# Kernel optimization log

Hardware: AMD Instinct MI355X
Metric: run time of the kernel (lower is better)

The kernel has to match this reference:

```python
import jax, jax.numpy as jnp
import numpy as np

B, S, H, NH = 2, 2048, 512, 8
DK = H // NH


def setup_inputs() -> dict:
    key = jax.random.key(0)
    ks = jax.random.split(key, 12)
    inp = {
        "query": jax.random.normal(ks[0], (B, S, H), dtype=jnp.float32),
        "key": jax.random.normal(ks[1], (B, S, H), dtype=jnp.float32),
        "value": jax.random.normal(ks[2], (B, S, H), dtype=jnp.float32),
        "bias": jax.random.normal(ks[3], (B, 1, S, S), dtype=jnp.float32),
        "mask": jax.random.randint(ks[4], (B, S), 0, 2, dtype=jnp.int32),
        "Wq": jax.random.normal(ks[5], (H, H), dtype=jnp.float32) * 0.02,
        "bq": jax.random.normal(ks[6], (H,), dtype=jnp.float32) * 0.02,
        "Wk": jax.random.normal(ks[7], (H, H), dtype=jnp.float32) * 0.02,
        "bk": jax.random.normal(ks[8], (H,), dtype=jnp.float32) * 0.02,
        "Wv": jax.random.normal(ks[9], (H, H), dtype=jnp.float32) * 0.02,
        "bv": jax.random.normal(ks[10], (H,), dtype=jnp.float32) * 0.02,
    }
    return inp


def reference(query, key, value, bias, mask, Wq, bq, Wk, bk, Wv, bv):
    b = query.shape[0]
    # torch nn.Linear: x @ W.T + b, then split heads -> [B, h, S, d_k]
    def proj(x, W, bb):
        y = x @ W.T + bb
        return y.reshape(b, -1, NH, DK).transpose(0, 2, 1, 3)

    q = proj(query, Wq, bq)
    k = proj(key, Wk, bk)
    v = proj(value, Wv, bv)

    score = jnp.einsum("bhqd,bhkd->bhqk", q, k) / np.sqrt(DK).astype(np.float32)
    # NOTE: the source swaps bias/mask when calling attention():
    #   the 0/1 mask is ADDED to the scores...
    mask_add = mask.reshape(b, 1, 1, -1).astype(score.dtype)
    score = score + mask_add
    #   ...and the float bias is used for the masked_fill (bias == 0 -> -1e30).
    score = jnp.where(bias == 0, jnp.asarray(-1e30, score.dtype), score)
    attn = jax.nn.softmax(score, axis=-1)  # dropout=None in the source call
    x = jnp.einsum("bhqk,bhkd->bhqd", attn, v)
    return x.transpose(0, 2, 1, 3).reshape(b, -1, NH * DK)
```

## Files before the change

kernel.cpp:

```cpp
#include <hip/hip_runtime.h>
#include <hip/hip_bf16.h>
#include <stdint.h>

#define B_  2
#define S_  2048
#define H_  512
#define NH_ 8
#define DK_ 64

typedef __bf16 bf16x8 __attribute__((ext_vector_type(8)));
typedef short  s16x4  __attribute__((ext_vector_type(4)));
typedef float  f32x4  __attribute__((ext_vector_type(4)));

static __device__ __forceinline__ uint32_t pk2(float a, float b) {
  __hip_bfloat162 h = __float22bfloat162_rn(float2{a, b});
  uint32_t u;
  __builtin_memcpy(&u, &h, 4);
  return u;
}
static __device__ __forceinline__ uint4 pkf8(float4 a, float4 b) {
  return uint4{pk2(a.x, a.y), pk2(a.z, a.w), pk2(b.x, b.y), pk2(b.z, b.w)};
}

static __device__ __forceinline__ f32x4 mfma_k16(s16x4 a, s16x4 b, f32x4 c) {
#if defined(__HIP_DEVICE_COMPILE__)
  return __builtin_amdgcn_mfma_f32_16x16x16bf16_1k(a, b, c, 0, 0, 0);
#else
  (void)a; (void)b;
  return c;
#endif
}

typedef const __attribute__((address_space(1))) uint32_t* gas_t;
typedef __attribute__((address_space(3))) uint32_t* las_t;
static __device__ __forceinline__ void cp16(const void* g, void* l) {
  __builtin_amdgcn_global_load_lds((gas_t)g, (las_t)l, 16, 0, 0);
}

__global__ __launch_bounds__(256) void prep_kernel(const float* __restrict__ bias,
                                                   const int* __restrict__ mask,
                                                   uint32_t* __restrict__ zc,
                                                   float* __restrict__ fmL) {
  int bid = blockIdx.x, t = threadIdx.x;
  if (bid < 4096) {
    size_t tid = (size_t)bid * 256 + t;
    const uint4* src = (const uint4*)(bias + tid * 8);
    uint4 a = src[0], b2 = src[1];
    bool z = ((a.x << 1) == 0u) | ((a.y << 1) == 0u) |
             ((a.z << 1) == 0u) | ((a.w << 1) == 0u) |
             ((b2.x << 1) == 0u) | ((b2.y << 1) == 0u) |
             ((b2.z << 1) == 0u) | ((b2.w << 1) == 0u);
    if (z) {
      size_t flat = tid * 8;
      int bb = (int)(flat >> 22);
      int q  = (int)(flat >> 11) & 2047;
      int k  = (int)flat & 2047;
      atomicOr(&zc[(bb * 32 + (q >> 6)) * 32 + (k >> 6)], 1u);
    }
  } else {
    const float LOG2E = 1.44269504088896340736f;
#pragma unroll
    for (int i = 0; i < 16; i++) {
      int idx = i * 256 + t;
      fmL[idx] = (float)mask[idx] * LOG2E;
    }
  }
}

struct ProjArgs {
  const float* X[3];
  const float* W[3];
  const float* Bv[3];
  uint16_t*    O[3];
};

__global__ __launch_bounds__(256) void proj_kernel(ProjArgs pa) {
  int bid = blockIdx.x;
  int mat = bid >> 8;
  int rem = bid & 255;
  int mtile = rem >> 3, dtile = rem & 7;
  int m0 = mtile * 128, n0 = dtile * 64;
  const float* X  = pa.X[mat];
  const float* Wt = pa.W[mat];
  const float* Bv = pa.Bv[mat];
  uint16_t*    O  = pa.O[mat];

  __shared__ uint16_t Xs[128][64];
  __shared__ uint16_t Ws[64][64];

  int t = threadIdx.x;
  int w = t >> 6, l = t & 63, lo = l & 15, g = l >> 4;
  int srow = t >> 1, shalf = t & 1;
  int wrow = t >> 2, wq = t & 3;

  const float* Xrow = X + (size_t)(m0 + srow) * 512 + shalf * 32;
  const float* Wrow = Wt + (size_t)(n0 + wrow) * 512 + wq * 16;

  f32x4 acc[2][4];
#pragma unroll
  for (int st = 0; st < 2; st++)
#pragma unroll
    for (int dt = 0; dt < 4; dt++) acc[st][dt] = (f32x4){0.f, 0.f, 0.f, 0.f};

  float4 xa[8], wa2[4];
  {
    const float4* sx = (const float4*)Xrow;
    const float4* sw = (const float4*)Wrow;
#pragma unroll
    for (int i = 0; i < 8; i++) xa[i] = sx[i];
#pragma unroll
    for (int i = 0; i < 4; i++) wa2[i] = sw[i];
  }

  for (int kb = 0; kb < 8; kb++) {
#pragma unroll
    for (int j = 0; j < 4; j++) {
      int s = (shalf * 4 + j) ^ (srow & 7);
      *(uint4*)&Xs[srow][s * 8] = pkf8(xa[2 * j], xa[2 * j + 1]);
    }
#pragma unroll
    for (int j = 0; j < 2; j++) {
      int s = (wq * 2 + j) ^ (wrow & 7);
      *(uint4*)&Ws[wrow][s * 8] = pkf8(wa2[2 * j], wa2[2 * j + 1]);
    }
    __syncthreads();
    if (kb < 7) {
      const float4* sx = (const float4*)(Xrow + (kb + 1) * 64);
      const float4* sw = (const float4*)(Wrow + (kb + 1) * 64);
#pragma unroll
      for (int i = 0; i < 8; i++) xa[i] = sx[i];
#pragma unroll
      for (int i = 0; i < 4; i++) wa2[i] = sw[i];
    }
#pragma unroll
    for (int kk = 0; kk < 2; kk++) {
      int seg = (kk * 4 + g) ^ (lo & 7);
      bf16x8 xf[2], wf[4];
#pragma unroll
      for (int st = 0; st < 2; st++)
        xf[st] = *(const bf16x8*)&Xs[w * 32 + st * 16 + lo][seg * 8];
#pragma unroll
      for (int dt = 0; dt < 4; dt++)
        wf[dt] = *(const bf16x8*)&Ws[dt * 16 + lo][seg * 8];
      if (mat < 2) {
#pragma unroll
        for (int st = 0; st < 2; st++)
#pragma unroll
          for (int dt = 0; dt < 4; dt++)
            acc[st][dt] = __builtin_amdgcn_mfma_f32_16x16x32_bf16(wf[dt], xf[st], acc[st][dt], 0, 0, 0);
      } else {
#pragma unroll
        for (int st = 0; st < 2; st++)
#pragma unroll
          for (int dt = 0; dt < 4; dt++)
            acc[st][dt] = __builtin_amdgcn_mfma_f32_16x16x32_bf16(xf[st], wf[dt], acc[st][dt], 0, 0, 0);
      }
    }
    __syncthreads();
  }

  if (mat < 2) {
    float scale = (mat == 0) ? 0.125f : 1.0f;
    float4 bv4[4];
#pragma unroll
    for (int dt = 0; dt < 4; dt++)
      bv4[dt] = *(const float4*)(Bv + n0 + dt * 16 + g * 4);
#pragma unroll
    for (int st = 0; st < 2; st++) {
      int ss = m0 + w * 32 + st * 16 + lo;
      int bb = ss >> 11, sIn = ss & 2047;
      uint16_t* obase = O + ((size_t)(bb * NH_ + dtile) * S_ + sIn) * DK_;
#pragma unroll
      for (int dt = 0; dt < 4; dt++) {
        float v0 = (acc[st][dt][0] + bv4[dt].x) * scale;
        float v1 = (acc[st][dt][1] + bv4[dt].y) * scale;
        float v2 = (acc[st][dt][2] + bv4[dt].z) * scale;
        float v3 = (acc[st][dt][3] + bv4[dt].w) * scale;
        uint2 pk{pk2(v0, v1), pk2(v2, v3)};
        *(uint2*)(obase + dt * 16 + g * 4) = pk;
      }
    }
  } else {
    float bval[4];
#pragma unroll
    for (int dt = 0; dt < 4; dt++) bval[dt] = Bv[n0 + dt * 16 + lo];
#pragma unroll
    for (int st = 0; st < 2; st++) {
      int m = m0 + w * 32 + st * 16 + g * 4;
      int bb = m >> 11, sIn = m & 2047;
#pragma unroll
      for (int dt = 0; dt < 4; dt++) {
        int dd = dt * 16 + lo;
        float v0 = acc[st][dt][0] + bval[dt];
        float v1 = acc[st][dt][1] + bval[dt];
        float v2 = acc[st][dt][2] + bval[dt];
        float v3 = acc[st][dt][3] + bval[dt];
        uint2 pk{pk2(v0, v1), pk2(v2, v3)};
        *(uint2*)(O + ((size_t)(bb * NH_ + dtile) * DK_ + dd) * S_ + sIn) = pk;
      }
    }
  }
}

__global__ __launch_bounds__(256, 2) void attn_kernel(
    const uint16_t* __restrict__ Qb, const uint16_t* __restrict__ Kb,
    const uint16_t* __restrict__ Vt, const uint32_t* __restrict__ zc,
    const float* __restrict__ fmL, const float* __restrict__ bias,
    float* __restrict__ out) {
  int bid = blockIdx.x;
  int bh = bid & 15, qtile = bid >> 4;
  int b = bh >> 3, h = bh & 7;
  int q0 = qtile * 64;
  int t = threadIdx.x;
  int w = t >> 6, l = t & 63, lo = l & 15, g = l >> 4;

  __shared__ __align__(16) char smem[32768];
  uint16_t* KsB = (uint16_t*)smem;
  uint16_t* VsB = (uint16_t*)(smem + 16384);

  const uint16_t* Qh = Qb + (size_t)bh * S_ * DK_;
  const uint16_t* Kh = Kb + (size_t)bh * S_ * DK_;
  const uint16_t* Vh = Vt + (size_t)bh * DK_ * S_;

  int lrow = l >> 3, lseg = (l & 7) ^ (lrow & 7);
  const uint16_t* kbase = Kh + (size_t)(w * 16 + lrow) * DK_ + lseg * 8;
  const uint16_t* vbase = Vh + (size_t)(w * 16 + lrow) * S_ + lseg * 8;
  uint16_t* kd0 = KsB + (w * 16) * 64;
  uint16_t* kd8 = KsB + (w * 16 + 8) * 64;
  uint16_t* vd0 = VsB + (w * 16) * 64;
  uint16_t* vd8 = VsB + (w * 16 + 8) * 64;

  bf16x8 qf[4][2];
#pragma unroll
  for (int qt = 0; qt < 4; qt++)
#pragma unroll
    for (int kk = 0; kk < 2; kk++)
      qf[qt][kk] = *(const bf16x8*)(Qh + (size_t)(q0 + qt * 16 + lo) * DK_ + kk * 32 + g * 8);

  f32x4 o[4][4];
#pragma unroll
  for (int dt = 0; dt < 4; dt++)
#pragma unroll
    for (int qt = 0; qt < 4; qt++) o[dt][qt] = (f32x4){0.f, 0.f, 0.f, 0.f};
  float ts[4] = {0.f, 0.f, 0.f, 0.f};

  const uint32_t* zcr = zc + ((b * 32 + qtile) << 5);
  const float* fmrow = fmL + b * S_ + w * 16 + g * 4;
  const float LOG2E = 1.44269504088896340736f;

  cp16(kbase, kd0);
  cp16(kbase + 512, kd8);
  cp16(vbase, vd0);
  cp16(vbase + 8 * S_, vd8);

  for (int kb = 0; kb < 32; kb++) {
    int cur = kb & 1;
    int k0 = kb * 64;
    float4 mv4 = *(const float4*)(fmrow + k0);
    uint32_t zci = zcr[kb];
    __syncthreads();
    if (kb + 1 < 32) {
      int kn = k0 + 64;
      int nb = (cur ^ 1) * 4096;
      cp16(kbase + (size_t)kn * 64, kd0 + nb);
      cp16(kbase + (size_t)kn * 64 + 512, kd8 + nb);
      cp16(vbase + kn, vd0 + nb);
      cp16(vbase + kn + 8 * S_, vd8 + nb);
    }
    const uint16_t* KsT = KsB + cur * 4096;
    const uint16_t* VsT = VsB + cur * 4096;

    s16x4 vf[4];
    {
      int s = (2 * w + (g >> 1)) ^ (lo & 7);
      int off = s * 8 + (g & 1) * 4;
#pragma unroll
      for (int dt = 0; dt < 4; dt++)
        vf[dt] = *(const s16x4*)(VsT + (dt * 16 + lo) * 64 + off);
    }
    bf16x8 kf[2];
#pragma unroll
    for (int kk = 0; kk < 2; kk++) {
      int s = (kk * 4 + g) ^ (lo & 7);
      kf[kk] = *(const bf16x8*)(KsT + (w * 16 + lo) * 64 + s * 8);
    }

    f32x4 c[4];
#pragma unroll
    for (int qt = 0; qt < 4; qt++) {
      f32x4 z = {0.f, 0.f, 0.f, 0.f};
      z = __builtin_amdgcn_mfma_f32_16x16x32_bf16(kf[0], qf[qt][0], z, 0, 0, 0);
      c[qt] = __builtin_amdgcn_mfma_f32_16x16x32_bf16(kf[1], qf[qt][1], z, 0, 0, 0);
    }

    float p[4][4];
    if (zci == 0u) {
#pragma unroll
      for (int qt = 0; qt < 4; qt++) {
        p[qt][0] = __builtin_amdgcn_exp2f(__builtin_fmaf(c[qt][0], LOG2E, mv4.x));
        p[qt][1] = __builtin_amdgcn_exp2f(__builtin_fmaf(c[qt][1], LOG2E, mv4.y));
        p[qt][2] = __builtin_amdgcn_exp2f(__builtin_fmaf(c[qt][2], LOG2E, mv4.z));
        p[qt][3] = __builtin_amdgcn_exp2f(__builtin_fmaf(c[qt][3], LOG2E, mv4.w));
      }
    } else {
#pragma unroll
      for (int qt = 0; qt < 4; qt++) {
        float4 bz = *(const float4*)(bias + ((size_t)(b * S_ + q0 + qt * 16 + lo)) * S_ + k0 + w * 16 + g * 4);
        p[qt][0] = (bz.x == 0.f) ? 0.f : __builtin_amdgcn_exp2f(__builtin_fmaf(c[qt][0], LOG2E, mv4.x));
        p[qt][1] = (bz.y == 0.f) ? 0.f : __builtin_amdgcn_exp2f(__builtin_fmaf(c[qt][1], LOG2E, mv4.y));
        p[qt][2] = (bz.z == 0.f) ? 0.f : __builtin_amdgcn_exp2f(__builtin_fmaf(c[qt][2], LOG2E, mv4.z));
        p[qt][3] = (bz.w == 0.f) ? 0.f : __builtin_amdgcn_exp2f(__builtin_fmaf(c[qt][3], LOG2E, mv4.w));
      }
    }

    s16x4 pf[4];
#pragma unroll
    for (int qt = 0; qt < 4; qt++) {
      ts[qt] += (p[qt][0] + p[qt][1]) + (p[qt][2] + p[qt][3]);
      union { s16x4 v; uint32_t u[2]; } uu;
      uu.u[0] = pk2(p[qt][0], p[qt][1]);
      uu.u[1] = pk2(p[qt][2], p[qt][3]);
      pf[qt] = uu.v;
    }

#pragma unroll
    for (int dt = 0; dt < 4; dt++)
#pragma unroll
      for (int qt = 0; qt < 4; qt++)
        o[dt][qt] = mfma_k16(vf[dt], pf[qt], o[dt][qt]);
  }

  float* OT = (float*)smem;
  float* LS = (float*)(smem + 17408);
#pragma unroll
  for (int qt = 0; qt < 4; qt++) {
    float v = ts[qt];
    v += __shfl_xor(v, 16);
    v += __shfl_xor(v, 32);
    ts[qt] = v;
  }
  __syncthreads();
  if (g == 0) {
#pragma unroll
    for (int qt = 0; qt < 4; qt++) LS[(w * 4 + qt) * 16 + lo] = ts[qt];
  }
#pragma unroll
  for (int ww = 0; ww < 4; ww++) {
    if (w == ww) {
#pragma unroll
      for (int dt = 0; dt < 4; dt++)
#pragma unroll
        for (int qt = 0; qt < 4; qt++)
#pragma unroll
          for (int r = 0; r < 4; r++) {
            int idx = (dt * 16 + g * 4 + r) * 68 + qt * 16 + lo;
            if (ww == 0) OT[idx] = o[dt][qt][r];
            else         OT[idx] += o[dt][qt][r];
          }
    }
    __syncthreads();
  }
  {
    int q = t >> 2, dseg = (t & 3) * 16;
    int qt2 = q >> 4, lo2 = q & 15;
    float lsum = LS[(0 * 4 + qt2) * 16 + lo2] + LS[(1 * 4 + qt2) * 16 + lo2] +
                 LS[(2 * 4 + qt2) * 16 + lo2] + LS[(3 * 4 + qt2) * 16 + lo2];
    float linv = 1.0f / fmaxf(lsum, 1e-30f);
    float* ob = out + ((size_t)(b * S_ + q0 + q)) * H_ + h * DK_ + dseg;
#pragma unroll
    for (int i = 0; i < 4; i++) {
      float4 v;
      v.x = OT[(dseg + i * 4 + 0) * 68 + q] * linv;
      v.y = OT[(dseg + i * 4 + 1) * 68 + q] * linv;
      v.z = OT[(dseg + i * 4 + 2) * 68 + q] * linv;
      v.w = OT[(dseg + i * 4 + 3) * 68 + q] * linv;
      *(float4*)(ob + i * 4) = v;
    }
  }
}

extern "C" void kernel_launch(void* const* d_in, const int* in_sizes, int n_in,
                              void* d_out, int out_size, void* d_ws, size_t ws_size,
                              hipStream_t stream) {
  const float* query = (const float*)d_in[0];
  const float* key   = (const float*)d_in[1];
  const float* value = (const float*)d_in[2];
  const float* bias  = (const float*)d_in[3];
  const int*   mask  = (const int*)d_in[4];
  const float* Wq = (const float*)d_in[5];
  const float* bq = (const float*)d_in[6];
  const float* Wk = (const float*)d_in[7];
  const float* bk = (const float*)d_in[8];
  const float* Wv = (const float*)d_in[9];
  const float* bv = (const float*)d_in[10];

  char* ws = (char*)d_ws;
  uint32_t* zcflags = (uint32_t*)ws;
  float*    fmL     = (float*)(ws + 8192);
  uint16_t* Qb = (uint16_t*)(ws + (size_t)(1 << 20));
  uint16_t* Kb = (uint16_t*)(ws + (size_t)(5 << 20));
  uint16_t* Vt = (uint16_t*)(ws + (size_t)(9 << 20));

  (void)hipMemsetAsync(zcflags, 0, 8192, stream);
  prep_kernel<<<4097, 256, 0, stream>>>(bias, mask, zcflags, fmL);

  ProjArgs pa;
  pa.X[0] = query; pa.X[1] = key; pa.X[2] = value;
  pa.W[0] = Wq;    pa.W[1] = Wk;  pa.W[2] = Wv;
  pa.Bv[0] = bq;   pa.Bv[1] = bk; pa.Bv[2] = bv;
  pa.O[0] = Qb;    pa.O[1] = Kb;  pa.O[2] = Vt;
  proj_kernel<<<768, 256, 0, stream>>>(pa);

  attn_kernel<<<512, 256, 0, stream>>>(Qb, Kb, Vt, zcflags, fmL, bias, (float*)d_out);
}
```

Baseline: 179.4 us.

## Fuse bias-zero scan into projection kernel and double attention key tile per block

Merges the bias-zero scan and mask prep into the projection launch, and drops the memset and atomics. Zero flags are now stored as per-row bitmasks built with wave ballots, then OR-reduced per query tile inside attention. The attention kernel moves to 512 threads that process 128-key blocks with larger LDS double buffers and a two-bank output reduction. This cuts launch count and per-iteration sync overhead, at the cost of 64KB of LDS per block and coarser zero-skip granularity (128 keys).

```diff
diff --git a/kernel.cpp b/kernel.cpp
--- a/kernel.cpp
+++ b/kernel.cpp
@@ -37,46 +37,54 @@
   __builtin_amdgcn_global_load_lds((gas_t)g, (las_t)l, 16, 0, 0);
 }
 
-__global__ __launch_bounds__(256) void prep_kernel(const float* __restrict__ bias,
-                                                   const int* __restrict__ mask,
-                                                   uint32_t* __restrict__ zc,
-                                                   float* __restrict__ fmL) {
-  int bid = blockIdx.x, t = threadIdx.x;
-  if (bid < 4096) {
-    size_t tid = (size_t)bid * 256 + t;
-    const uint4* src = (const uint4*)(bias + tid * 8);
-    uint4 a = src[0], b2 = src[1];
-    bool z = ((a.x << 1) == 0u) | ((a.y << 1) == 0u) |
-             ((a.z << 1) == 0u) | ((a.w << 1) == 0u) |
-             ((b2.x << 1) == 0u) | ((b2.y << 1) == 0u) |
-             ((b2.z << 1) == 0u) | ((b2.w << 1) == 0u);
-    if (z) {
-      size_t flat = tid * 8;
-      int bb = (int)(flat >> 22);
-      int q  = (int)(flat >> 11) & 2047;
-      int k  = (int)flat & 2047;
-      atomicOr(&zc[(bb * 32 + (q >> 6)) * 32 + (k >> 6)], 1u);
-    }
-  } else {
-    const float LOG2E = 1.44269504088896340736f;
-#pragma unroll
-    for (int i = 0; i < 16; i++) {
-      int idx = i * 256 + t;
-      fmL[idx] = (float)mask[idx] * LOG2E;
-    }
-  }
-}
-
 struct ProjArgs {
   const float* X[3];
   const float* W[3];
   const float* Bv[3];
   uint16_t*    O[3];
+  const float* bias;
+  const int*   mask;
+  uint32_t*    zrow;
+  float*       fmL;
 };
 
-__global__ __launch_bounds__(256) void proj_kernel(ProjArgs pa) {
-  int bid = blockIdx.x;
-  int mat = bid >> 8;
+__global__ __launch_bounds__(256) void prep_proj_kernel(ProjArgs pa) {
+  __shared__ __align__(16) char psm[24640];
+  int bid = blockIdx.x, t = threadIdx.x;
+
+  if (bid >= 768) {
+    if (bid < 4864) {
+      int r = bid - 768;
+      uint32_t* wbuf = (uint32_t*)psm;
+      const uint4* src = (const uint4*)(pa.bias + (size_t)r * 2048 + t * 8);
+      uint4 a = src[0], b2 = src[1];
+      bool z = ((a.x << 1) == 0u) | ((a.y << 1) == 0u) |
+               ((a.z << 1) == 0u) | ((a.w << 1) == 0u) |
+               ((b2.x << 1) == 0u) | ((b2.y << 1) == 0u) |
+               ((b2.z << 1) == 0u) | ((b2.w << 1) == 0u);
+      uint64_t m = __ballot(z);
+      if ((t & 63) == 0) {
+        uint32_t bits = 0;
+#pragma unroll
+        for (int c = 0; c < 8; c++)
+          bits |= (uint32_t)(((m >> (8 * c)) & 0xFFull) != 0ull) << c;
+        wbuf[t >> 6] = bits;
+      }
+      __syncthreads();
+      if (t == 0)
+        pa.zrow[r] = wbuf[0] | (wbuf[1] << 8) | (wbuf[2] << 16) | (wbuf[3] << 24);
+    } else {
+      const float LOG2E = 1.44269504088896340736f;
+#pragma unroll
+      for (int i = 0; i < 16; i++) {
+        int idx = i * 256 + t;
+        pa.fmL[idx] = (float)pa.mask[idx] * LOG2E;
+      }
+    }
+    return;
+  }
+
+  int mat = bid / 256;
   int rem = bid & 255;
   int mtile = rem >> 3, dtile = rem & 7;
   int m0 = mtile * 128, n0 = dtile * 64;
@@ -85,10 +93,9 @@
   const float* Bv = pa.Bv[mat];
   uint16_t*    O  = pa.O[mat];
 
-  __shared__ uint16_t Xs[128][64];
-  __shared__ uint16_t Ws[64][64];
-
-  int t = threadIdx.x;
+  uint16_t (*Xs)[64] = (uint16_t (*)[64])psm;
+  uint16_t (*Ws)[64] = (uint16_t (*)[64])(psm + 16384);
+
   int w = t >> 6, l = t & 63, lo = l & 15, g = l >> 4;
   int srow = t >> 1, shalf = t & 1;
   int wrow = t >> 2, wq = t & 3;
@@ -202,9 +209,9 @@
   }
 }
 
-__global__ __launch_bounds__(256, 2) void attn_kernel(
+__global__ __launch_bounds__(512, 4) void attn_kernel(
     const uint16_t* __restrict__ Qb, const uint16_t* __restrict__ Kb,
-    const uint16_t* __restrict__ Vt, const uint32_t* __restrict__ zc,
+    const uint16_t* __restrict__ Vt, const uint32_t* __restrict__ zrow,
     const float* __restrict__ fmL, const float* __restrict__ bias,
     float* __restrict__ out) {
   int bid = blockIdx.x;
@@ -214,21 +221,28 @@
   int t = threadIdx.x;
   int w = t >> 6, l = t & 63, lo = l & 15, g = l >> 4;
 
-  __shared__ __align__(16) char smem[32768];
+  __shared__ __align__(16) char smem[65536];
   uint16_t* KsB = (uint16_t*)smem;
-  uint16_t* VsB = (uint16_t*)(smem + 16384);
+  uint16_t* VsB = (uint16_t*)(smem + 32768);
 
   const uint16_t* Qh = Qb + (size_t)bh * S_ * DK_;
   const uint16_t* Kh = Kb + (size_t)bh * S_ * DK_;
   const uint16_t* Vh = Vt + (size_t)bh * DK_ * S_;
 
-  int lrow = l >> 3, lseg = (l & 7) ^ (lrow & 7);
+  int lrow = l >> 3, lseg = (l & 7) ^ lrow;
   const uint16_t* kbase = Kh + (size_t)(w * 16 + lrow) * DK_ + lseg * 8;
-  const uint16_t* vbase = Vh + (size_t)(w * 16 + lrow) * S_ + lseg * 8;
   uint16_t* kd0 = KsB + (w * 16) * 64;
   uint16_t* kd8 = KsB + (w * 16 + 8) * 64;
-  uint16_t* vd0 = VsB + (w * 16) * 64;
-  uint16_t* vd8 = VsB + (w * 16 + 8) * 64;
+  int vrow0 = w * 4 + (l >> 4);
+  int vrow1 = 32 + w * 4 + (l >> 4);
+  const uint16_t* vb0 = Vh + (size_t)vrow0 * S_ + (((l & 15) ^ (vrow0 & 15)) * 8);
+  const uint16_t* vb1 = Vh + (size_t)vrow1 * S_ + (((l & 15) ^ (vrow1 & 15)) * 8);
+  uint16_t* vd0 = VsB + (w * 4) * 128;
+  uint16_t* vd1 = VsB + (32 + w * 4) * 128;
+
+  uint32_t zall = zrow[(b << 11) + q0 + l];
+#pragma unroll
+  for (int s = 1; s < 64; s <<= 1) zall |= __shfl_xor(zall, s);
 
   bf16x8 qf[4][2];
 #pragma unroll
@@ -244,45 +258,44 @@
     for (int qt = 0; qt < 4; qt++) o[dt][qt] = (f32x4){0.f, 0.f, 0.f, 0.f};
   float ts[4] = {0.f, 0.f, 0.f, 0.f};
 
-  const uint32_t* zcr = zc + ((b * 32 + qtile) << 5);
   const float* fmrow = fmL + b * S_ + w * 16 + g * 4;
   const float LOG2E = 1.44269504088896340736f;
 
   cp16(kbase, kd0);
-  cp16(kbase + 512, kd8);
-  cp16(vbase, vd0);
-  cp16(vbase + 8 * S_, vd8);
-
-  for (int kb = 0; kb < 32; kb++) {
+  cp16(kbase + 8 * DK_, kd8);
+  cp16(vb0, vd0);
+  cp16(vb1, vd1);
+
+  for (int kb = 0; kb < 16; kb++) {
     int cur = kb & 1;
-    int k0 = kb * 64;
+    int k0 = kb * 128;
     float4 mv4 = *(const float4*)(fmrow + k0);
-    uint32_t zci = zcr[kb];
     __syncthreads();
-    if (kb + 1 < 32) {
-      int kn = k0 + 64;
-      int nb = (cur ^ 1) * 4096;
-      cp16(kbase + (size_t)kn * 64, kd0 + nb);
-      cp16(kbase + (size_t)kn * 64 + 512, kd8 + nb);
-      cp16(vbase + kn, vd0 + nb);
-      cp16(vbase + kn + 8 * S_, vd8 + nb);
-    }
-    const uint16_t* KsT = KsB + cur * 4096;
-    const uint16_t* VsT = VsB + cur * 4096;
+    if (kb + 1 < 16) {
+      int kn = k0 + 128;
+      int nb = (cur ^ 1) * 8192;
+      cp16(kbase + (size_t)kn * DK_, kd0 + nb);
+      cp16(kbase + (size_t)kn * DK_ + 8 * DK_, kd8 + nb);
+      cp16(vb0 + kn, vd0 + nb);
+      cp16(vb1 + kn, vd1 + nb);
+    }
+    const uint16_t* KsT = KsB + cur * 8192;
+    const uint16_t* VsT = VsB + cur * 8192;
 
     s16x4 vf[4];
     {
-      int s = (2 * w + (g >> 1)) ^ (lo & 7);
-      int off = s * 8 + (g & 1) * 4;
-#pragma unroll
-      for (int dt = 0; dt < 4; dt++)
-        vf[dt] = *(const s16x4*)(VsT + (dt * 16 + lo) * 64 + off);
+      int sl = 2 * w + (g >> 1);
+#pragma unroll
+      for (int dt = 0; dt < 4; dt++) {
+        int sp = sl ^ lo;
+        vf[dt] = *(const s16x4*)(VsT + (dt * 16 + lo) * 128 + sp * 8 + (g & 1) * 4);
+      }
     }
     bf16x8 kf[2];
 #pragma unroll
     for (int kk = 0; kk < 2; kk++) {
-      int s = (kk * 4 + g) ^ (lo & 7);
-      kf[kk] = *(const bf16x8*)(KsT + (w * 16 + lo) * 64 + s * 8);
+      int sp = (kk * 4 + g) ^ (lo & 7);
+      kf[kk] = *(const bf16x8*)(KsT + (w * 16 + lo) * 64 + sp * 8);
     }
 
     f32x4 c[4];
@@ -294,7 +307,7 @@
     }
 
     float p[4][4];
-    if (zci == 0u) {
+    if (((zall >> (2 * kb)) & 3u) == 0u) {
 #pragma unroll
       for (int qt = 0; qt < 4; qt++) {
         p[qt][0] = __builtin_amdgcn_exp2f(__builtin_fmaf(c[qt][0], LOG2E, mv4.x));
@@ -330,8 +343,9 @@
         o[dt][qt] = mfma_k16(vf[dt], pf[qt], o[dt][qt]);
   }
 
-  float* OT = (float*)smem;
-  float* LS = (float*)(smem + 17408);
+  float* OTA = (float*)smem;
+  float* OTB = (float*)(smem + 17664);
+  float* LS  = (float*)(smem + 35328);
 #pragma unroll
   for (int qt = 0; qt < 4; qt++) {
     float v = ts[qt];
@@ -344,16 +358,17 @@
 #pragma unroll
     for (int qt = 0; qt < 4; qt++) LS[(w * 4 + qt) * 16 + lo] = ts[qt];
   }
+  float* OT = (w < 4) ? OTA : OTB;
 #pragma unroll
   for (int ww = 0; ww < 4; ww++) {
-    if (w == ww) {
+    if ((w & 3) == ww) {
 #pragma unroll
       for (int dt = 0; dt < 4; dt++)
 #pragma unroll
         for (int qt = 0; qt < 4; qt++)
 #pragma unroll
           for (int r = 0; r < 4; r++) {
-            int idx = (dt * 16 + g * 4 + r) * 68 + qt * 16 + lo;
+            int idx = (dt * 16 + g * 4 + r) * 69 + qt * 16 + lo;
             if (ww == 0) OT[idx] = o[dt][qt][r];
             else         OT[idx] += o[dt][qt][r];
           }
@@ -361,19 +376,20 @@
     __syncthreads();
   }
   {
-    int q = t >> 2, dseg = (t & 3) * 16;
+    int q = t >> 3, dseg = (t & 7) * 8;
     int qt2 = q >> 4, lo2 = q & 15;
-    float lsum = LS[(0 * 4 + qt2) * 16 + lo2] + LS[(1 * 4 + qt2) * 16 + lo2] +
-                 LS[(2 * 4 + qt2) * 16 + lo2] + LS[(3 * 4 + qt2) * 16 + lo2];
+    float lsum = 0.f;
+#pragma unroll
+    for (int ww = 0; ww < 8; ww++) lsum += LS[(ww * 4 + qt2) * 16 + lo2];
     float linv = 1.0f / fmaxf(lsum, 1e-30f);
     float* ob = out + ((size_t)(b * S_ + q0 + q)) * H_ + h * DK_ + dseg;
 #pragma unroll
-    for (int i = 0; i < 4; i++) {
+    for (int i = 0; i < 2; i++) {
       float4 v;
-      v.x = OT[(dseg + i * 4 + 0) * 68 + q] * linv;
-      v.y = OT[(dseg + i * 4 + 1) * 68 + q] * linv;
-      v.z = OT[(dseg + i * 4 + 2) * 68 + q] * linv;
-      v.w = OT[(dseg + i * 4 + 3) * 68 + q] * linv;
+      v.x = (OTA[(dseg + i * 4 + 0) * 69 + q] + OTB[(dseg + i * 4 + 0) * 69 + q]) * linv;
+      v.y = (OTA[(dseg + i * 4 + 1) * 69 + q] + OTB[(dseg + i * 4 + 1) * 69 + q]) * linv;
+      v.z = (OTA[(dseg + i * 4 + 2) * 69 + q] + OTB[(dseg + i * 4 + 2) * 69 + q]) * linv;
+      v.w = (OTA[(dseg + i * 4 + 3) * 69 + q] + OTB[(dseg + i * 4 + 3) * 69 + q]) * linv;
       *(float4*)(ob + i * 4) = v;
     }
   }
@@ -395,21 +411,21 @@
   const float* bv = (const float*)d_in[10];
 
   char* ws = (char*)d_ws;
-  uint32_t* zcflags = (uint32_t*)ws;
-  float*    fmL     = (float*)(ws + 8192);
+  uint32_t* zrow = (uint32_t*)ws;
+  float*    fmL  = (float*)(ws + 16384);
   uint16_t* Qb = (uint16_t*)(ws + (size_t)(1 << 20));
   uint16_t* Kb = (uint16_t*)(ws + (size_t)(5 << 20));
   uint16_t* Vt = (uint16_t*)(ws + (size_t)(9 << 20));
-
-  (void)hipMemsetAsync(zcflags, 0, 8192, stream);
-  prep_kernel<<<4097, 256, 0, stream>>>(bias, mask, zcflags, fmL);
 
   ProjArgs pa;
   pa.X[0] = query; pa.X[1] = key; pa.X[2] = value;
   pa.W[0] = Wq;    pa.W[1] = Wk;  pa.W[2] = Wv;
   pa.Bv[0] = bq;   pa.Bv[1] = bk; pa.Bv[2] = bv;
   pa.O[0] = Qb;    pa.O[1] = Kb;  pa.O[2] = Vt;
-  proj_kernel<<<768, 256, 0, stream>>>(pa);
-
-  attn_kernel<<<512, 256, 0, stream>>>(Qb, Kb, Vt, zcflags, fmL, bias, (float*)d_out);
-}
+  pa.bias = bias;  pa.mask = mask;
+  pa.zrow = zrow;  pa.fmL = fmL;
+
+  prep_proj_kernel<<<4865, 256, 0, stream>>>(pa);
+
+  attn_kernel<<<512, 512, 0, stream>>>(Qb, Kb, Vt, zrow, fmL, bias, (float*)d_out);
+}
```

Result: slower. 233.2 us (+30.0%).
